# Optimization experiments

Measured on AMD Instinct MI355X. Metric: run time of the kernel, lower is better.

Reference implementation:

```python
import jax, jax.numpy as jnp
import numpy as np

H = 8        # hidden_size
T = 609      # seq_size
IN = 5       # input feature dim
B = 2048     # batch


def _lstm_layer(x, Wih, Whh, bih, bhh):
    """PyTorch-compatible single-layer LSTM, batch_first. x: [B, T, I].
    Gate order i, f, g, o; zero initial (h, c)."""
    b = x.shape[0]
    h_dim = Wih.shape[0] // 4
    bias = bih + bhh

    def step(carry, xt):
        h, c = carry
        gates = xt @ Wih.T + h @ Whh.T + bias          # [B, 4H]
        i, f, g, o = jnp.split(gates, 4, axis=-1)
        i = jax.nn.sigmoid(i)
        f = jax.nn.sigmoid(f)
        g = jnp.tanh(g)
        o = jax.nn.sigmoid(o)
        c = f * c + i * g
        h = o * jnp.tanh(c)
        return (h, c), h

    h0 = jnp.zeros((b, h_dim), x.dtype)
    (_, _), ys = jax.lax.scan(step, (h0, h0), jnp.swapaxes(x, 0, 1))  # ys: [T, B, H]
    return jnp.swapaxes(ys, 0, 1)                                      # [B, T, H]


def setup_inputs() -> dict:
    key = jax.random.key(0)
    ks = jax.random.split(key, 20)
    s_lstm = 1.0 / np.sqrt(H)   # PyTorch LSTM init scale

    def u(k, shape, s):
        return jax.random.uniform(k, shape, jnp.float32, -s, s)

    inp = {"x": jax.random.normal(ks[0], (B, T, IN), jnp.float32)}
    # LSTM layer 1 (input 5), layers 2-3 (input H)
    ins = [IN, H, H]
    for l in range(3):
        k0, k1, k2, k3 = jax.random.split(ks[1 + l], 4)
        inp[f"Wih{l+1}"] = u(k0, (4 * H, ins[l]), s_lstm)
        inp[f"Whh{l+1}"] = u(k1, (4 * H, H), s_lstm)
        inp[f"bih{l+1}"] = u(k2, (4 * H,), s_lstm)
        inp[f"bhh{l+1}"] = u(k3, (4 * H,), s_lstm)
    # MLP head
    d_in = H * T  # 4872
    dims = [(4096, d_in), (1024, 4096), (T, 1024)]
    for i, (o, ii) in enumerate(dims):
        s = 1.0 / np.sqrt(ii)
        k0, k1 = jax.random.split(ks[10 + i], 2)
        inp[f"W{i+1}"] = u(k0, (o, ii), s)
        inp[f"b{i+1}"] = u(k1, (o,), s)
    return inp


def reference(x, Wih1, Whh1, bih1, bhh1, Wih2, Whh2, bih2, bhh2,
              Wih3, Whh3, bih3, bhh3, W1, b1, W2, b2, W3, b3):
    out = _lstm_layer(x, Wih1, Whh1, bih1, bhh1)
    out = _lstm_layer(out, Wih2, Whh2, bih2, bhh2)
    out = _lstm_layer(out, Wih3, Whh3, bih3, bhh3)
    out = out.reshape(x.shape[0], -1)              # [B, T*H]
    out = jax.nn.relu(out @ W1.T + b1)
    out = jax.nn.relu(out @ W2.T + b2)
    out = out @ W3.T + b3                          # [B, T]
    return out
```

## Files before the change

### kernel.cpp

```cpp
#include <hip/hip_runtime.h>
#include <hip/hip_bf16.h>

typedef __attribute__((ext_vector_type(8))) short short8;
typedef __attribute__((ext_vector_type(4))) float floatx4;
typedef unsigned short u16;

#define T_SZ 609
#define K1V  4872
#define K1P  4896
#define RD   4

static __device__ __forceinline__ u16 f2bf(float f) {
    union { float f; unsigned u; } a; a.f = f;
    unsigned r = a.u + 0x7FFF + ((a.u >> 16) & 1);
    return (u16)(r >> 16);
}

static __device__ __forceinline__ void gload_lds16(const u16* g, u16* l) {
    __builtin_amdgcn_global_load_lds(
        (const __attribute__((address_space(1))) void*)g,
        (__attribute__((address_space(3))) void*)l, 16, 0, 0);
}

#define WG_LOAD(p)     __hip_atomic_load((p), __ATOMIC_ACQUIRE, __HIP_MEMORY_SCOPE_WORKGROUP)
#define WG_STORE(p, v) __hip_atomic_store((p), (v), __ATOMIC_RELEASE, __HIP_MEMORY_SCOPE_WORKGROUP)

__global__ __launch_bounds__(256) void cvt_kernel(const float* __restrict__ s,
                                                  u16* __restrict__ d, int n) {
    int i = (blockIdx.x * 256 + threadIdx.x) * 8;
    if (i < n) {
        float4 a = *(const float4*)(s + i);
        float4 b = *(const float4*)(s + i + 4);
        u16 o[8] = { f2bf(a.x), f2bf(a.y), f2bf(a.z), f2bf(a.w),
                     f2bf(b.x), f2bf(b.y), f2bf(b.z), f2bf(b.w) };
        *(uint4*)(d + i) = *(const uint4*)o;
    }
}

__global__ __launch_bounds__(256) void cvt_pad_kernel(const float* __restrict__ s,
                                                      u16* __restrict__ d,
                                                      int R, int K, int Kp) {
    int chunk = blockIdx.x * 256 + threadIdx.x;
    int cpr = Kp >> 3;
    int r = chunk / cpr;
    int c = (chunk - r * cpr) << 3;
    u16 o[8] = {0, 0, 0, 0, 0, 0, 0, 0};
    if (r < R && c < K) {
        const float* p = s + (size_t)r * K + c;
        float4 a = *(const float4*)p;
        float4 b = *(const float4*)(p + 4);
        o[0] = f2bf(a.x); o[1] = f2bf(a.y); o[2] = f2bf(a.z); o[3] = f2bf(a.w);
        o[4] = f2bf(b.x); o[5] = f2bf(b.y); o[6] = f2bf(b.z); o[7] = f2bf(b.w);
    }
    *(uint4*)&d[(size_t)r * Kp + c] = *(const uint4*)o;
}

__global__ __launch_bounds__(192) void lstm3_kernel(
    const float* __restrict__ x,
    const float* __restrict__ Wih1, const float* __restrict__ Whh1,
    const float* __restrict__ bih1, const float* __restrict__ bhh1,
    const float* __restrict__ Wih2, const float* __restrict__ Whh2,
    const float* __restrict__ bih2, const float* __restrict__ bhh2,
    const float* __restrict__ Wih3, const float* __restrict__ Whh3,
    const float* __restrict__ bih3, const float* __restrict__ bhh3,
    u16* __restrict__ A1)
{
    __shared__ __align__(16) float xs[2 * T_SZ * 5];
    __shared__ __align__(16) float r1[RD * 16], r2[RD * 16], r3[RD * 16];
    __shared__ int p1, p2, c2, c3;

    const int tid = threadIdx.x;
    const int b0  = blockIdx.x * 2;

    const float* xg = x + (size_t)b0 * (T_SZ * 5);
    for (int i = tid; i < 2 * T_SZ * 5; i += 192) xs[i] = xg[i];
    if (tid == 0) { p1 = 0; p2 = 0; c2 = 0; c3 = 0; }
    if (tid < 48) {
        int r = tid / 24, c = tid - r * 24;
        A1[(size_t)(b0 + r) * K1P + K1V + c] = 0;
    }
    __syncthreads();

    const int lane = tid & 63, wid = tid >> 6;
    const int gi   = lane & 31;
    const int rh   = lane >> 5;
    const int jj   = gi & 7;
    const int gt   = gi >> 3;
    const int base = lane & 32;

    const float am = (gt == 2) ? -2.f : -1.f;
    const float aa = (gt == 2) ?  2.f :  1.f;
    const float ab = (gt == 2) ? -1.f :  0.f;

    auto lstep = [&](float a, float& c) -> float {
        float e = __expf(am * a);
        float v = __builtin_fmaf(aa, __fdividef(1.f, 1.f + e), ab);
        float vi = __shfl(v, base + jj,      64);
        float vf = __shfl(v, base + 8 + jj,  64);
        float vg = __shfl(v, base + 16 + jj, 64);
        float vo = __shfl(v, base + 24 + jj, 64);
        c = __builtin_fmaf(vf, c, vi * vg);
        float ec = __expf(-2.f * __builtin_fabsf(c));
        float th = (1.f - ec) * __fdividef(1.f, 1.f + ec);
        return vo * __builtin_copysignf(th, c);
    };

    auto dot8 = [&](const float* hp, const float* w, float& a, float& b) {
        float4 h0 = *(const float4*)hp;
        float4 h1 = *(const float4*)(hp + 4);
        a = __builtin_fmaf(w[0], h0.x, a); b = __builtin_fmaf(w[1], h0.y, b);
        a = __builtin_fmaf(w[2], h0.z, a); b = __builtin_fmaf(w[3], h0.w, b);
        a = __builtin_fmaf(w[4], h1.x, a); b = __builtin_fmaf(w[5], h1.y, b);
        a = __builtin_fmaf(w[6], h1.z, a); b = __builtin_fmaf(w[7], h1.w, b);
    };

    if (wid == 0) {
        float wi[5], wh[8];
#pragma unroll
        for (int k = 0; k < 5; ++k) wi[k] = Wih1[gi * 5 + k];
#pragma unroll
        for (int k = 0; k < 8; ++k) wh[k] = Whh1[gi * 8 + k];
        const float bs = bih1[gi] + bhh1[gi];
        const float* xr = &xs[rh * (T_SZ * 5)];
        float cst = 0.f;
        for (int t = 0; t < T_SZ; ++t) {
            float a = bs, b = 0.f;
#pragma unroll
            for (int k = 0; k < 5; ++k) a = __builtin_fmaf(wi[k], xr[t * 5 + k], a);
            if (t > 0) dot8(&r1[((t - 1) & (RD - 1)) * 16 + rh * 8], wh, a, b);
            float h = lstep(a + b, cst);
            if (t >= RD) while (WG_LOAD(&c2) < t - (RD - 1)) {}
            if (gi < 8) r1[(t & (RD - 1)) * 16 + rh * 8 + jj] = h;
            if (lane == 0) WG_STORE(&p1, t + 1);
        }
    } else if (wid == 1) {
        float wi[8], wh[8];
#pragma unroll
        for (int k = 0; k < 8; ++k) { wi[k] = Wih2[gi * 8 + k]; wh[k] = Whh2[gi * 8 + k]; }
        const float bs = bih2[gi] + bhh2[gi];
        float cst = 0.f;
        for (int t = 0; t < T_SZ; ++t) {
            while (WG_LOAD(&p1) < t + 1) {}
            float a = bs, b = 0.f;
            dot8(&r1[(t & (RD - 1)) * 16 + rh * 8], wi, a, b);
            if (lane == 0) WG_STORE(&c2, t + 1);
            if (t > 0) dot8(&r2[((t - 1) & (RD - 1)) * 16 + rh * 8], wh, a, b);
            float h = lstep(a + b, cst);
            if (t >= RD) while (WG_LOAD(&c3) < t - (RD - 1)) {}
            if (gi < 8) r2[(t & (RD - 1)) * 16 + rh * 8 + jj] = h;
            if (lane == 0) WG_STORE(&p2, t + 1);
        }
    } else {
        float wi[8], wh[8];
#pragma unroll
        for (int k = 0; k < 8; ++k) { wi[k] = Wih3[gi * 8 + k]; wh[k] = Whh3[gi * 8 + k]; }
        const float bs = bih3[gi] + bhh3[gi];
        float cst = 0.f;
        u16* outp = A1 + (size_t)(b0 + rh) * K1P;
        for (int t = 0; t < T_SZ; ++t) {
            while (WG_LOAD(&p2) < t + 1) {}
            float a = bs, b = 0.f;
            dot8(&r2[(t & (RD - 1)) * 16 + rh * 8], wi, a, b);
            if (lane == 0) WG_STORE(&c3, t + 1);
            if (t > 0) dot8(&r3[((t - 1) & (RD - 1)) * 16 + rh * 8], wh, a, b);
            float h = lstep(a + b, cst);
            if (gi < 8) {
                r3[(t & (RD - 1)) * 16 + rh * 8 + jj] = h;
                outp[t * 8 + jj] = f2bf(h);
            }
        }
    }
}

template<int BM, int BN, bool RELU, bool NGUARD, bool OUTF32>
__global__ __launch_bounds__(256) void gemm_bt(
    const u16* __restrict__ A, int lda,
    const u16* __restrict__ B, int ldb,
    const float* __restrict__ bias,
    void* __restrict__ Cv, int ldc, int N, int K)
{
    constexpr int WM = BM / 2, WN = BN / 2;
    constexpr int TM = WM / 16, TN = WN / 16;
    __shared__ u16 As[BM * 32];
    __shared__ u16 Bs[BN * 32];

    const int tid = threadIdx.x;
    const int bm  = blockIdx.y * BM;
    const int bn  = blockIdx.x * BN;
    const int l   = tid & 63, w = tid >> 6;
    const int wr  = w >> 1, wc = w & 1;
    const int lr  = l & 15, q = l >> 4;
    const int lrow = l >> 2;
    const int lcol = (l & 3) << 3;

    floatx4 acc[TM][TN];
#pragma unroll
    for (int i = 0; i < TM; ++i)
#pragma unroll
        for (int j = 0; j < TN; ++j) acc[i][j] = (floatx4){0.f, 0.f, 0.f, 0.f};

    const u16* Ab = A + (size_t)bm * lda;
    const u16* Bb = B + (size_t)bn * ldb;

    for (int k0 = 0; k0 < K; k0 += 32) {
#pragma unroll
        for (int i = 0; i < BM / 64; ++i) {
            int r0 = w * (BM / 4) + i * 16;
            gload_lds16(Ab + (size_t)(r0 + lrow) * lda + k0 + lcol, &As[r0 * 32]);
        }
#pragma unroll
        for (int i = 0; i < BN / 64; ++i) {
            int r0 = w * (BN / 4) + i * 16;
            gload_lds16(Bb + (size_t)(r0 + lrow) * ldb + k0 + lcol, &Bs[r0 * 32]);
        }
        __syncthreads();

        short8 fa[TM], fb[TN];
#pragma unroll
        for (int i = 0; i < TM; ++i)
            fa[i] = *(const short8*)&As[(wr * WM + i * 16 + lr) * 32 + q * 8];
#pragma unroll
        for (int j = 0; j < TN; ++j)
            fb[j] = *(const short8*)&Bs[(wc * WN + j * 16 + lr) * 32 + q * 8];
#pragma unroll
        for (int i = 0; i < TM; ++i)
#pragma unroll
            for (int j = 0; j < TN; ++j)
                acc[i][j] = __builtin_amdgcn_mfma_f32_16x16x32_bf16(fa[i], fb[j], acc[i][j], 0, 0, 0);
        __syncthreads();
    }

#pragma unroll
    for (int j = 0; j < TN; ++j) {
        int n = bn + wc * WN + j * 16 + lr;
        bool nok = (!NGUARD) || (n < N);
        float bv = nok ? bias[n] : 0.f;
#pragma unroll
        for (int i = 0; i < TM; ++i) {
            int m0r = bm + wr * WM + i * 16 + q * 4;
#pragma unroll
            for (int r = 0; r < 4; ++r) {
                float vv = acc[i][j][r] + bv;
                if (RELU) vv = fmaxf(vv, 0.f);
                if (nok) {
                    size_t idx = (size_t)(m0r + r) * ldc + n;
                    if (OUTF32) ((float*)Cv)[idx] = vv;
                    else        ((u16*)Cv)[idx] = f2bf(vv);
                }
            }
        }
    }
}

extern "C" void kernel_launch(void* const* d_in, const int* in_sizes, int n_in,
                              void* d_out, int out_size, void* d_ws, size_t ws_size,
                              hipStream_t stream)
{
    const float* x    = (const float*)d_in[0];
    const float* Wih1 = (const float*)d_in[1];
    const float* Whh1 = (const float*)d_in[2];
    const float* bih1 = (const float*)d_in[3];
    const float* bhh1 = (const float*)d_in[4];
    const float* Wih2 = (const float*)d_in[5];
    const float* Whh2 = (const float*)d_in[6];
    const float* bih2 = (const float*)d_in[7];
    const float* bhh2 = (const float*)d_in[8];
    const float* Wih3 = (const float*)d_in[9];
    const float* Whh3 = (const float*)d_in[10];
    const float* bih3 = (const float*)d_in[11];
    const float* bhh3 = (const float*)d_in[12];
    const float* W1 = (const float*)d_in[13];
    const float* b1 = (const float*)d_in[14];
    const float* W2 = (const float*)d_in[15];
    const float* b2 = (const float*)d_in[16];
    const float* W3 = (const float*)d_in[17];
    const float* b3 = (const float*)d_in[18];

    u16* A1  = (u16*)d_ws;
    u16* A2  = A1  + (size_t)2048 * K1P;
    u16* A3  = A2  + (size_t)2048 * 4096;
    u16* W1b = A3  + (size_t)2048 * 1024;
    u16* W2b = W1b + (size_t)4096 * K1P;
    u16* W3b = W2b + (size_t)1024 * 4096;

    cvt_pad_kernel<<<9792, 256, 0, stream>>>(W1, W1b, 4096, K1V, K1P);
    cvt_kernel<<<2048, 256, 0, stream>>>(W2, W2b, 1024 * 4096);
    cvt_pad_kernel<<<320, 256, 0, stream>>>(W3, W3b, T_SZ, 1024, 1024);

    lstm3_kernel<<<1024, 192, 0, stream>>>(x, Wih1, Whh1, bih1, bhh1,
                                           Wih2, Whh2, bih2, bhh2,
                                           Wih3, Whh3, bih3, bhh3, A1);

    gemm_bt<128, 128, true, false, false><<<dim3(32, 16), 256, 0, stream>>>(
        A1, K1P, W1b, K1P, b1, A2, 4096, 4096, K1P);

    gemm_bt<64, 128, true, false, false><<<dim3(8, 32), 256, 0, stream>>>(
        A2, 4096, W2b, 4096, b2, A3, 1024, 1024, 4096);

    gemm_bt<64, 128, false, true, true><<<dim3(5, 32), 256, 0, stream>>>(
        A3, 1024, W3b, 1024, b3, d_out, T_SZ, T_SZ, 1024);
}
```

Measured before the change: 699.6 us.

## Map one lane per hidden unit computing all four gates, 8 batch rows per block

The LSTM kernel now assigns each lane one hidden unit of one batch row and computes all four gates in registers, removing the cross-lane shuffles. This packs 8 batch rows per 64-lane wave instead of 2, so the launch shrinks from 1024 to 256 blocks. Layer 1's input projection for the next step is computed ahead to overlap with the current step. Each lane now does four times the FMAs and transcendentals per step and holds more weight registers. With only 256 blocks the GPU may be underoccupied, which lengthens the serial recurrence on each block.

After: 701.5 us. No clear change (+0.3%).

```diff
diff --git a/kernel.cpp b/kernel.cpp
--- a/kernel.cpp
+++ b/kernel.cpp
@@ -65,109 +65,201 @@
     const float* __restrict__ bih3, const float* __restrict__ bhh3,
     u16* __restrict__ A1)
 {
-    __shared__ __align__(16) float xs[2 * T_SZ * 5];
-    __shared__ __align__(16) float r1[RD * 16], r2[RD * 16], r3[RD * 16];
-    __shared__ int p1, p2, c2, c3;
+    __shared__ __align__(16) float xs[8 * T_SZ * 5];
+    __shared__ __align__(16) float r1[RD * 64], r2[RD * 64], r3[RD * 64];
+    __shared__ int s_p1, s_p2, s_c2, s_c3;
 
     const int tid = threadIdx.x;
-    const int b0  = blockIdx.x * 2;
-
-    const float* xg = x + (size_t)b0 * (T_SZ * 5);
-    for (int i = tid; i < 2 * T_SZ * 5; i += 192) xs[i] = xg[i];
-    if (tid == 0) { p1 = 0; p2 = 0; c2 = 0; c3 = 0; }
-    if (tid < 48) {
+    const int b0  = blockIdx.x * 8;
+
+    const float4* xg4 = (const float4*)(x + (size_t)b0 * (T_SZ * 5));
+    float4* xs4 = (float4*)xs;
+    for (int i = tid; i < (8 * T_SZ * 5) / 4; i += 192) xs4[i] = xg4[i];
+    if (tid == 0) { s_p1 = 0; s_p2 = 0; s_c2 = 0; s_c3 = 0; }
+    {
         int r = tid / 24, c = tid - r * 24;
-        A1[(size_t)(b0 + r) * K1P + K1V + c] = 0;
+        if (r < 8) A1[(size_t)(b0 + r) * K1P + K1V + c] = 0;
     }
     __syncthreads();
 
     const int lane = tid & 63, wid = tid >> 6;
-    const int gi   = lane & 31;
-    const int rh   = lane >> 5;
-    const int jj   = gi & 7;
-    const int gt   = gi >> 3;
-    const int base = lane & 32;
-
-    const float am = (gt == 2) ? -2.f : -1.f;
-    const float aa = (gt == 2) ?  2.f :  1.f;
-    const float ab = (gt == 2) ? -1.f :  0.f;
-
-    auto lstep = [&](float a, float& c) -> float {
-        float e = __expf(am * a);
-        float v = __builtin_fmaf(aa, __fdividef(1.f, 1.f + e), ab);
-        float vi = __shfl(v, base + jj,      64);
-        float vf = __shfl(v, base + 8 + jj,  64);
-        float vg = __shfl(v, base + 16 + jj, 64);
-        float vo = __shfl(v, base + 24 + jj, 64);
-        c = __builtin_fmaf(vf, c, vi * vg);
+    const int row  = lane >> 3;
+    const int jj   = lane & 7;
+    const int rb   = row * 8;
+
+    auto gates = [&](float p0, float p1, float p2, float p3, float& c) -> float {
+        float ei = __expf(-p0); float i_ = __fdividef(1.f, 1.f + ei);
+        float ef = __expf(-p1); float f_ = __fdividef(1.f, 1.f + ef);
+        float eg = __expf(-2.f * __builtin_fabsf(p2));
+        float g_ = __builtin_copysignf((1.f - eg) * __fdividef(1.f, 1.f + eg), p2);
+        float eo = __expf(-p3); float o_ = __fdividef(1.f, 1.f + eo);
+        c = __builtin_fmaf(f_, c, i_ * g_);
         float ec = __expf(-2.f * __builtin_fabsf(c));
         float th = (1.f - ec) * __fdividef(1.f, 1.f + ec);
-        return vo * __builtin_copysignf(th, c);
+        return o_ * __builtin_copysignf(th, c);
     };
 
-    auto dot8 = [&](const float* hp, const float* w, float& a, float& b) {
-        float4 h0 = *(const float4*)hp;
-        float4 h1 = *(const float4*)(hp + 4);
-        a = __builtin_fmaf(w[0], h0.x, a); b = __builtin_fmaf(w[1], h0.y, b);
-        a = __builtin_fmaf(w[2], h0.z, a); b = __builtin_fmaf(w[3], h0.w, b);
-        a = __builtin_fmaf(w[4], h1.x, a); b = __builtin_fmaf(w[5], h1.y, b);
-        a = __builtin_fmaf(w[6], h1.z, a); b = __builtin_fmaf(w[7], h1.w, b);
-    };
-
     if (wid == 0) {
-        float wi[5], wh[8];
-#pragma unroll
-        for (int k = 0; k < 5; ++k) wi[k] = Wih1[gi * 5 + k];
-#pragma unroll
-        for (int k = 0; k < 8; ++k) wh[k] = Whh1[gi * 8 + k];
-        const float bs = bih1[gi] + bhh1[gi];
-        const float* xr = &xs[rh * (T_SZ * 5)];
-        float cst = 0.f;
+        float wi[4][5], wh[4][8], bs[4];
+#pragma unroll
+        for (int g = 0; g < 4; ++g) {
+#pragma unroll
+            for (int k = 0; k < 5; ++k) wi[g][k] = Wih1[(g * 8 + jj) * 5 + k];
+#pragma unroll
+            for (int k = 0; k < 8; ++k) wh[g][k] = Whh1[(g * 8 + jj) * 8 + k];
+            bs[g] = bih1[g * 8 + jj] + bhh1[g * 8 + jj];
+        }
+        const float* xr = &xs[row * (T_SZ * 5)];
+        float c = 0.f;
+        float xa0, xa1, xa2, xa3;
+        {
+            float v0 = xr[0], v1 = xr[1], v2 = xr[2], v3 = xr[3], v4 = xr[4];
+            xa0 = bs[0]; xa1 = bs[1]; xa2 = bs[2]; xa3 = bs[3];
+            xa0 = __builtin_fmaf(wi[0][0], v0, xa0); xa1 = __builtin_fmaf(wi[1][0], v0, xa1);
+            xa2 = __builtin_fmaf(wi[2][0], v0, xa2); xa3 = __builtin_fmaf(wi[3][0], v0, xa3);
+            xa0 = __builtin_fmaf(wi[0][1], v1, xa0); xa1 = __builtin_fmaf(wi[1][1], v1, xa1);
+            xa2 = __builtin_fmaf(wi[2][1], v1, xa2); xa3 = __builtin_fmaf(wi[3][1], v1, xa3);
+            xa0 = __builtin_fmaf(wi[0][2], v2, xa0); xa1 = __builtin_fmaf(wi[1][2], v2, xa1);
+            xa2 = __builtin_fmaf(wi[2][2], v2, xa2); xa3 = __builtin_fmaf(wi[3][2], v2, xa3);
+            xa0 = __builtin_fmaf(wi[0][3], v3, xa0); xa1 = __builtin_fmaf(wi[1][3], v3, xa1);
+            xa2 = __builtin_fmaf(wi[2][3], v3, xa2); xa3 = __builtin_fmaf(wi[3][3], v3, xa3);
+            xa0 = __builtin_fmaf(wi[0][4], v4, xa0); xa1 = __builtin_fmaf(wi[1][4], v4, xa1);
+            xa2 = __builtin_fmaf(wi[2][4], v4, xa2); xa3 = __builtin_fmaf(wi[3][4], v4, xa3);
+        }
         for (int t = 0; t < T_SZ; ++t) {
-            float a = bs, b = 0.f;
-#pragma unroll
-            for (int k = 0; k < 5; ++k) a = __builtin_fmaf(wi[k], xr[t * 5 + k], a);
-            if (t > 0) dot8(&r1[((t - 1) & (RD - 1)) * 16 + rh * 8], wh, a, b);
-            float h = lstep(a + b, cst);
-            if (t >= RD) while (WG_LOAD(&c2) < t - (RD - 1)) {}
-            if (gi < 8) r1[(t & (RD - 1)) * 16 + rh * 8 + jj] = h;
-            if (lane == 0) WG_STORE(&p1, t + 1);
+            float p0 = xa0, p1 = xa1, p2 = xa2, p3 = xa3;
+            if (t > 0) {
+                const float* hp = &r1[((t - 1) & (RD - 1)) * 64 + rb];
+                float4 h0 = *(const float4*)hp;
+                float4 h1 = *(const float4*)(hp + 4);
+#pragma unroll
+                for (int g = 0; g < 4; ++g) {
+                    float* pp = (g == 0) ? &p0 : (g == 1) ? &p1 : (g == 2) ? &p2 : &p3;
+                    float a = *pp;
+                    a = __builtin_fmaf(wh[g][0], h0.x, a); a = __builtin_fmaf(wh[g][1], h0.y, a);
+                    a = __builtin_fmaf(wh[g][2], h0.z, a); a = __builtin_fmaf(wh[g][3], h0.w, a);
+                    a = __builtin_fmaf(wh[g][4], h1.x, a); a = __builtin_fmaf(wh[g][5], h1.y, a);
+                    a = __builtin_fmaf(wh[g][6], h1.z, a); a = __builtin_fmaf(wh[g][7], h1.w, a);
+                    *pp = a;
+                }
+            }
+            if (t + 1 < T_SZ) {
+                const float* xn = xr + (t + 1) * 5;
+                float v0 = xn[0], v1 = xn[1], v2 = xn[2], v3 = xn[3], v4 = xn[4];
+                xa0 = bs[0]; xa1 = bs[1]; xa2 = bs[2]; xa3 = bs[3];
+                xa0 = __builtin_fmaf(wi[0][0], v0, xa0); xa1 = __builtin_fmaf(wi[1][0], v0, xa1);
+                xa2 = __builtin_fmaf(wi[2][0], v0, xa2); xa3 = __builtin_fmaf(wi[3][0], v0, xa3);
+                xa0 = __builtin_fmaf(wi[0][1], v1, xa0); xa1 = __builtin_fmaf(wi[1][1], v1, xa1);
+                xa2 = __builtin_fmaf(wi[2][1], v1, xa2); xa3 = __builtin_fmaf(wi[3][1], v1, xa3);
+                xa0 = __builtin_fmaf(wi[0][2], v2, xa0); xa1 = __builtin_fmaf(wi[1][2], v2, xa1);
+                xa2 = __builtin_fmaf(wi[2][2], v2, xa2); xa3 = __builtin_fmaf(wi[3][2], v2, xa3);
+                xa0 = __builtin_fmaf(wi[0][3], v3, xa0); xa1 = __builtin_fmaf(wi[1][3], v3, xa1);
+                xa2 = __builtin_fmaf(wi[2][3], v3, xa2); xa3 = __builtin_fmaf(wi[3][3], v3, xa3);
+                xa0 = __builtin_fmaf(wi[0][4], v4, xa0); xa1 = __builtin_fmaf(wi[1][4], v4, xa1);
+                xa2 = __builtin_fmaf(wi[2][4], v4, xa2); xa3 = __builtin_fmaf(wi[3][4], v4, xa3);
+            }
+            float h = gates(p0, p1, p2, p3, c);
+            if (t >= RD) while (WG_LOAD(&s_c2) < t - (RD - 1)) {}
+            r1[(t & (RD - 1)) * 64 + rb + jj] = h;
+            if (lane == 0) WG_STORE(&s_p1, t + 1);
         }
     } else if (wid == 1) {
-        float wi[8], wh[8];
-#pragma unroll
-        for (int k = 0; k < 8; ++k) { wi[k] = Wih2[gi * 8 + k]; wh[k] = Whh2[gi * 8 + k]; }
-        const float bs = bih2[gi] + bhh2[gi];
-        float cst = 0.f;
+        float wi[4][8], wh[4][8], bs[4];
+#pragma unroll
+        for (int g = 0; g < 4; ++g) {
+#pragma unroll
+            for (int k = 0; k < 8; ++k) {
+                wi[g][k] = Wih2[(g * 8 + jj) * 8 + k];
+                wh[g][k] = Whh2[(g * 8 + jj) * 8 + k];
+            }
+            bs[g] = bih2[g * 8 + jj] + bhh2[g * 8 + jj];
+        }
+        float c = 0.f;
         for (int t = 0; t < T_SZ; ++t) {
-            while (WG_LOAD(&p1) < t + 1) {}
-            float a = bs, b = 0.f;
-            dot8(&r1[(t & (RD - 1)) * 16 + rh * 8], wi, a, b);
-            if (lane == 0) WG_STORE(&c2, t + 1);
-            if (t > 0) dot8(&r2[((t - 1) & (RD - 1)) * 16 + rh * 8], wh, a, b);
-            float h = lstep(a + b, cst);
-            if (t >= RD) while (WG_LOAD(&c3) < t - (RD - 1)) {}
-            if (gi < 8) r2[(t & (RD - 1)) * 16 + rh * 8 + jj] = h;
-            if (lane == 0) WG_STORE(&p2, t + 1);
+            while (WG_LOAD(&s_p1) < t + 1) {}
+            const float* ip = &r1[(t & (RD - 1)) * 64 + rb];
+            float4 i0 = *(const float4*)ip;
+            float4 i1 = *(const float4*)(ip + 4);
+            float p0 = bs[0], p1 = bs[1], p2 = bs[2], p3 = bs[3];
+#pragma unroll
+            for (int g = 0; g < 4; ++g) {
+                float* pp = (g == 0) ? &p0 : (g == 1) ? &p1 : (g == 2) ? &p2 : &p3;
+                float a = *pp;
+                a = __builtin_fmaf(wi[g][0], i0.x, a); a = __builtin_fmaf(wi[g][1], i0.y, a);
+                a = __builtin_fmaf(wi[g][2], i0.z, a); a = __builtin_fmaf(wi[g][3], i0.w, a);
+                a = __builtin_fmaf(wi[g][4], i1.x, a); a = __builtin_fmaf(wi[g][5], i1.y, a);
+                a = __builtin_fmaf(wi[g][6], i1.z, a); a = __builtin_fmaf(wi[g][7], i1.w, a);
+                *pp = a;
+            }
+            if (lane == 0) WG_STORE(&s_c2, t + 1);
+            if (t > 0) {
+                const float* hp = &r2[((t - 1) & (RD - 1)) * 64 + rb];
+                float4 h0 = *(const float4*)hp;
+                float4 h1 = *(const float4*)(hp + 4);
+#pragma unroll
+                for (int g = 0; g < 4; ++g) {
+                    float* pp = (g == 0) ? &p0 : (g == 1) ? &p1 : (g == 2) ? &p2 : &p3;
+                    float a = *pp;
+                    a = __builtin_fmaf(wh[g][0], h0.x, a); a = __builtin_fmaf(wh[g][1], h0.y, a);
+                    a = __builtin_fmaf(wh[g][2], h0.z, a); a = __builtin_fmaf(wh[g][3], h0.w, a);
+                    a = __builtin_fmaf(wh[g][4], h1.x, a); a = __builtin_fmaf(wh[g][5], h1.y, a);
+                    a = __builtin_fmaf(wh[g][6], h1.z, a); a = __builtin_fmaf(wh[g][7], h1.w, a);
+                    *pp = a;
+                }
+            }
+            float h = gates(p0, p1, p2, p3, c);
+            if (t >= RD) while (WG_LOAD(&s_c3) < t - (RD - 1)) {}
+            r2[(t & (RD - 1)) * 64 + rb + jj] = h;
+            if (lane == 0) WG_STORE(&s_p2, t + 1);
         }
     } else {
-        float wi[8], wh[8];
-#pragma unroll
-        for (int k = 0; k < 8; ++k) { wi[k] = Wih3[gi * 8 + k]; wh[k] = Whh3[gi * 8 + k]; }
-        const float bs = bih3[gi] + bhh3[gi];
-        float cst = 0.f;
-        u16* outp = A1 + (size_t)(b0 + rh) * K1P;
+        float wi[4][8], wh[4][8], bs[4];
+#pragma unroll
+        for (int g = 0; g < 4; ++g) {
+#pragma unroll
+            for (int k = 0; k < 8; ++k) {
+                wi[g][k] = Wih3[(g * 8 + jj) * 8 + k];
+                wh[g][k] = Whh3[(g * 8 + jj) * 8 + k];
+            }
+            bs[g] = bih3[g * 8 + jj] + bhh3[g * 8 + jj];
+        }
+        float c = 0.f;
+        u16* outp = A1 + (size_t)(b0 + row) * K1P;
         for (int t = 0; t < T_SZ; ++t) {
-            while (WG_LOAD(&p2) < t + 1) {}
-            float a = bs, b = 0.f;
-            dot8(&r2[(t & (RD - 1)) * 16 + rh * 8], wi, a, b);
-            if (lane == 0) WG_STORE(&c3, t + 1);
-            if (t > 0) dot8(&r3[((t - 1) & (RD - 1)) * 16 + rh * 8], wh, a, b);
-            float h = lstep(a + b, cst);
-            if (gi < 8) {
-                r3[(t & (RD - 1)) * 16 + rh * 8 + jj] = h;
-                outp[t * 8 + jj] = f2bf(h);
-            }
+            while (WG_LOAD(&s_p2) < t + 1) {}
+            const float* ip = &r2[(t & (RD - 1)) * 64 + rb];
+            float4 i0 = *(const float4*)ip;
+            float4 i1 = *(const float4*)(ip + 4);
+            float p0 = bs[0], p1 = bs[1], p2 = bs[2], p3 = bs[3];
+#pragma unroll
+            for (int g = 0; g < 4; ++g) {
+                float* pp = (g == 0) ? &p0 : (g == 1) ? &p1 : (g == 2) ? &p2 : &p3;
+                float a = *pp;
+                a = __builtin_fmaf(wi[g][0], i0.x, a); a = __builtin_fmaf(wi[g][1], i0.y, a);
+                a = __builtin_fmaf(wi[g][2], i0.z, a); a = __builtin_fmaf(wi[g][3], i0.w, a);
+                a = __builtin_fmaf(wi[g][4], i1.x, a); a = __builtin_fmaf(wi[g][5], i1.y, a);
+                a = __builtin_fmaf(wi[g][6], i1.z, a); a = __builtin_fmaf(wi[g][7], i1.w, a);
+                *pp = a;
+            }
+            if (lane == 0) WG_STORE(&s_c3, t + 1);
+            if (t > 0) {
+                const float* hp = &r3[((t - 1) & (RD - 1)) * 64 + rb];
+                float4 h0 = *(const float4*)hp;
+                float4 h1 = *(const float4*)(hp + 4);
+#pragma unroll
+                for (int g = 0; g < 4; ++g) {
+                    float* pp = (g == 0) ? &p0 : (g == 1) ? &p1 : (g == 2) ? &p2 : &p3;
+                    float a = *pp;
+                    a = __builtin_fmaf(wh[g][0], h0.x, a); a = __builtin_fmaf(wh[g][1], h0.y, a);
+                    a = __builtin_fmaf(wh[g][2], h0.z, a); a = __builtin_fmaf(wh[g][3], h0.w, a);
+                    a = __builtin_fmaf(wh[g][4], h1.x, a); a = __builtin_fmaf(wh[g][5], h1.y, a);
+                    a = __builtin_fmaf(wh[g][6], h1.z, a); a = __builtin_fmaf(wh[g][7], h1.w, a);
+                    *pp = a;
+                }
+            }
+            float h = gates(p0, p1, p2, p3, c);
+            r3[(t & (RD - 1)) * 64 + rb + jj] = h;
+            outp[t * 8 + jj] = f2bf(h);
         }
     }
 }
@@ -287,9 +379,9 @@
     cvt_kernel<<<2048, 256, 0, stream>>>(W2, W2b, 1024 * 4096);
     cvt_pad_kernel<<<320, 256, 0, stream>>>(W3, W3b, T_SZ, 1024, 1024);
 
-    lstm3_kernel<<<1024, 192, 0, stream>>>(x, Wih1, Whh1, bih1, bhh1,
-                                           Wih2, Whh2, bih2, bhh2,
-                                           Wih3, Whh3, bih3, bhh3, A1);
+    lstm3_kernel<<<256, 192, 0, stream>>>(x, Wih1, Whh1, bih1, bhh1,
+                                          Wih2, Whh2, bih2, bhh2,
+                                          Wih3, Whh3, bih3, bhh3, A1);
 
     gemm_bt<128, 128, true, false, false><<<dim3(32, 16), 256, 0, stream>>>(
         A1, K1P, W1b, K1P, b1, A2, 4096, 4096, K1P);
```
